# Performance work log

Hardware: AMD Instinct MI355X
Metric: run time of the kernel (lower is better)

## Reference

```python
import jax, jax.numpy as jnp
import numpy as np

N_NODES = 50000
KEEP_PROB = 0.5  # dropout = 0.5


def setup_inputs() -> dict:
    key = jax.random.key(0)
    k1, k2, k3, k4, k5 = jax.random.split(key, 5)
    S, E, DIN, DOUT = 2, 800000, 512, 128
    x = jax.random.normal(k1, (N_NODES, DIN), dtype=jnp.float32)
    weights = jax.random.normal(k2, (S, DIN, DOUT), dtype=jnp.float32) * (1.0 / np.sqrt(DIN))
    adj_rows = jax.random.randint(k3, (S, E), 0, N_NODES, dtype=jnp.int32)
    adj_cols = jax.random.randint(k4, (S, E), 0, N_NODES, dtype=jnp.int32)
    adj_vals = jax.random.uniform(k5, (S, E), dtype=jnp.float32)
    return {"x": x, "weights": weights, "adj_rows": adj_rows,
            "adj_cols": adj_cols, "adj_vals": adj_vals}


def reference(x, weights, adj_rows, adj_cols, adj_vals):
    # Dropout (TF semantics: mask and scale by 1/keep_prob), fixed key for determinism.
    mask = (jax.random.uniform(jax.random.key(42), x.shape) < KEEP_PROB)
    xd = x * mask.astype(x.dtype) / KEEP_PROB
    # Dense GEMM per support: pre_sup[s] = dropout(x) @ W_s  -> [S, N, Dout]
    pre_sup = jnp.einsum('nd,sdo->sno', xd, weights)
    # SpMM per support: out[s] = A_s @ pre_sup[s] with A_s in COO form.
    def spmm(rows, cols, vals, h):
        return jax.ops.segment_sum(vals[:, None] * h[cols], rows,
                                   num_segments=N_NODES)
    out = jax.vmap(spmm)(adj_rows, adj_cols, adj_vals, pre_sup)  # [S, N, Dout]
    return jax.nn.relu(out)
```

## Files before the change

kernel.cpp:

```cpp
#include <hip/hip_runtime.h>
#include <stdint.h>

#define N_NODES 50000
#define DIN     512
#define DOUT    128
#define NSUP    2
#define EDGES   800000
#define NEDGE   (NSUP * EDGES)
#define NROWS   (NSUP * N_NODES)
#define NB      782
#define CH      8192
#define NCH     ((NEDGE + CH - 1) / CH)
#define EPT     16
#define SCAP    4096
#define NMASKW  ((N_NODES * DIN) / 32)
#define NMB     1563
#define NWC     256

typedef __attribute__((ext_vector_type(8))) short short8;
typedef __attribute__((ext_vector_type(4))) float f32x4;

__device__ __forceinline__ uint32_t rotl32(uint32_t v, uint32_t d) {
  return (v << d) | (v >> (32u - d));
}

__device__ __forceinline__ void threefry2x32(uint32_t x0, uint32_t x1,
                                             uint32_t& o0, uint32_t& o1) {
  const uint32_t ks0 = 0u;
  const uint32_t ks1 = 42u;
  const uint32_t ks2 = 0u ^ 42u ^ 0x1BD11BDAu;
  x0 += ks0; x1 += ks1;
#define TF_R(r) { x0 += x1; x1 = rotl32(x1, (r)); x1 ^= x0; }
  TF_R(13) TF_R(15) TF_R(26) TF_R(6)
  x0 += ks1; x1 += ks2 + 1u;
  TF_R(17) TF_R(29) TF_R(16) TF_R(24)
  x0 += ks2; x1 += ks0 + 2u;
  TF_R(13) TF_R(15) TF_R(26) TF_R(6)
  x0 += ks0; x1 += ks1 + 3u;
  TF_R(17) TF_R(29) TF_R(16) TF_R(24)
  x0 += ks1; x1 += ks2 + 4u;
  TF_R(13) TF_R(15) TF_R(26) TF_R(6)
  x0 += ks2; x1 += ks0 + 5u;
#undef TF_R
  o0 = x0; o1 = x1;
}

__device__ __forceinline__ bool keep_mask(uint32_t idx) {
  uint32_t o0, o1;
  threefry2x32(0u, idx, o0, o1);
  return ((o0 ^ o1) >> 31) == 0u;
}

__device__ __forceinline__ uint32_t pack_bf16x2(float a, float b) {
  uint32_t ua = __float_as_uint(a), ub = __float_as_uint(b);
  ua += 0x7fffu + ((ua >> 16) & 1u);
  ub += 0x7fffu + ((ub >> 16) & 1u);
  return (ua >> 16) | (ub & 0xffff0000u);
}

__device__ __forceinline__ uint32_t bf16rne(float f) {
  uint32_t u = __float_as_uint(f);
  u += 0x7fffu + ((u >> 16) & 1u);
  return u >> 16;
}

__global__ __launch_bounds__(512) void fused_pre(
    const int* __restrict__ rows, const float* __restrict__ w,
    uint32_t* __restrict__ maskbuf, int* __restrict__ gcnt,
    unsigned short* __restrict__ b16t) {
  const int t  = threadIdx.x;
  const int bb = blockIdx.x;
  if (bb < NCH) {
    __shared__ int hist[NB];
    for (int b = t; b < NB; b += 512) hist[b] = 0;
    __syncthreads();
    int e0 = bb * CH;
#pragma unroll
    for (int i = 0; i < EPT; ++i) {
      int e = e0 + i * 512 + t;
      if (e < NEDGE) {
        int s = (e >= EDGES) ? 1 : 0;
        int grow = s * N_NODES + rows[e];
        atomicAdd(&hist[grow >> 7], 1);
      }
    }
    __syncthreads();
    for (int b = t; b < NB; b += 512)
      if (hist[b]) atomicAdd(&gcnt[b], hist[b]);
  } else if (bb < NCH + NMB) {
    int wid = (bb - NCH) * 512 + t;
    if (wid < NMASKW) {
      uint32_t base = (uint32_t)wid * 32u;
      uint32_t m = 0u;
#pragma unroll 8
      for (int j = 0; j < 32; ++j)
        m |= (keep_mask(base + j) ? 1u : 0u) << j;
      maskbuf[wid] = m;
    }
  } else {
    int i = (bb - NCH - NMB) * 512 + t;
    if (i < NSUP * DIN * DOUT) {
      int s   = i >> 16;
      int rem = i & 65535;
      int k   = rem >> 7;
      int o   = rem & 127;
      b16t[(size_t)(s * DOUT + o) * DIN + k] = (unsigned short)bf16rne(w[i]);
    }
  }
}

__global__ __launch_bounds__(512) void gemm_mfma2(
    const float* __restrict__ x, const uint32_t* __restrict__ maskbuf,
    const unsigned short* __restrict__ b16t,
    unsigned short* __restrict__ pre16) {
  __shared__ unsigned short As[128 * 64];
  __shared__ unsigned short Bs[256 * 64];
  const int t    = threadIdx.x;
  const int lane = t & 63;
  const int w    = t >> 6;
  const int wr   = w >> 2;
  const int wc   = w & 3;
  const int m0   = blockIdx.x * 128;

  f32x4 acc[4][4];
#pragma unroll
  for (int i = 0; i < 4; ++i)
#pragma unroll
    for (int j = 0; j < 4; ++j) acc[i][j] = (f32x4){0.f, 0.f, 0.f, 0.f};

  for (int kc = 0; kc < DIN; kc += 64) {
    __syncthreads();
#pragma unroll
    for (int i = 0; i < 2; ++i) {
      int slot = i * 512 + t;
      int row  = slot >> 3;
      int k8   = (slot & 7) * 8;
      int grow = m0 + row;
      union { uint32_t u[4]; short8 s; } pk;
      if (grow < N_NODES) {
        uint32_t b8 = (uint32_t)grow * DIN + (uint32_t)(kc + k8);
        const float4* src = reinterpret_cast<const float4*>(x + b8);
        float4 v0 = src[0], v1 = src[1];
        float f[8] = {v0.x, v0.y, v0.z, v0.w, v1.x, v1.y, v1.z, v1.w};
        uint32_t bits = maskbuf[b8 >> 5] >> (b8 & 31u);
#pragma unroll
        for (int q = 0; q < 8; ++q)
          f[q] = ((bits >> q) & 1u) ? f[q] * 2.0f : 0.0f;
#pragma unroll
        for (int q = 0; q < 4; ++q) pk.u[q] = pack_bf16x2(f[2 * q], f[2 * q + 1]);
      } else {
#pragma unroll
        for (int q = 0; q < 4; ++q) pk.u[q] = 0u;
      }
      *reinterpret_cast<short8*>(&As[(row * 64 + k8) ^ ((row & 7) << 3)]) = pk.s;
    }
#pragma unroll
    for (int i = 0; i < 4; ++i) {
      int slot = i * 512 + t;
      int col  = slot >> 3;
      int k8   = (slot & 7) * 8;
      short8 v = *reinterpret_cast<const short8*>(
          b16t + (size_t)col * DIN + kc + k8);
      *reinterpret_cast<short8*>(&Bs[(col * 64 + k8) ^ ((col & 7) << 3)]) = v;
    }
    __syncthreads();

    short8 af[4][2], bf[2][4];
#pragma unroll
    for (int mf = 0; mf < 4; ++mf)
#pragma unroll
      for (int kk = 0; kk < 2; ++kk) {
        int row = wr * 64 + mf * 16 + (lane & 15);
        int idx = (row * 64 + kk * 32 + (lane >> 4) * 8) ^ ((row & 7) << 3);
        af[mf][kk] = *reinterpret_cast<const short8*>(&As[idx]);
      }
#pragma unroll
    for (int kk = 0; kk < 2; ++kk)
#pragma unroll
      for (int nf = 0; nf < 4; ++nf) {
        int col = wc * 64 + nf * 16 + (lane & 15);
        int idx = (col * 64 + kk * 32 + (lane >> 4) * 8) ^ ((col & 7) << 3);
        bf[kk][nf] = *reinterpret_cast<const short8*>(&Bs[idx]);
      }
#pragma unroll
    for (int mf = 0; mf < 4; ++mf)
#pragma unroll
      for (int nf = 0; nf < 4; ++nf)
#pragma unroll
        for (int kk = 0; kk < 2; ++kk)
          acc[mf][nf] = __builtin_amdgcn_mfma_f32_16x16x32_bf16(
              af[mf][kk], bf[kk][nf], acc[mf][nf], 0, 0, 0);
  }

#pragma unroll
  for (int mf = 0; mf < 4; ++mf) {
    int rbase = m0 + wr * 64 + mf * 16 + ((lane >> 4) * 4);
#pragma unroll
    for (int nf = 0; nf < 4; ++nf) {
      int col = wc * 64 + nf * 16 + (lane & 15);
      int s = col >> 7, o = col & 127;
#pragma unroll
      for (int q = 0; q < 4; ++q) {
        int row = rbase + q;
        if (row < N_NODES)
          pre16[(size_t)(s * N_NODES + row) * DOUT + o] =
              (unsigned short)bf16rne(acc[mf][nf][q]);
      }
    }
  }
}

__global__ __launch_bounds__(1024) void scan782(const int* __restrict__ gcnt,
                                                int* __restrict__ bstart,
                                                int* __restrict__ gcursor) {
  __shared__ int sm[1024];
  int t = threadIdx.x;
  int c = (t < NB) ? gcnt[t] : 0;
  sm[t] = c;
  __syncthreads();
  for (int d = 1; d < 1024; d <<= 1) {
    int v = sm[t];
    int a = (t >= d) ? sm[t - d] : 0;
    __syncthreads();
    sm[t] = v + a;
    __syncthreads();
  }
  if (t < NB) {
    int ex = sm[t] - c;
    bstart[t] = ex;
    gcursor[t] = ex;
  }
  if (t == NB - 1) bstart[NB] = sm[t];
}

__global__ __launch_bounds__(512) void bin_scatter(
    const int* __restrict__ rows, const int* __restrict__ cols,
    const float* __restrict__ vals, int* __restrict__ gcursor,
    uint64_t* __restrict__ binned) {
  __shared__ uint32_t hist[NB];
  __shared__ uint32_t hexcl[NB];
  __shared__ uint32_t sbase[NB];
  __shared__ uint32_t scanb[512];
  __shared__ uint64_t ordered[CH];
  __shared__ uint16_t bk16[CH];
  int t = threadIdx.x;
  for (int b = t; b < NB; b += 512) hist[b] = 0;
  __syncthreads();
  int e0 = blockIdx.x * CH;
  uint32_t key[EPT], rank[EPT], bkt[EPT], vbits[EPT];
#pragma unroll
  for (int i = 0; i < EPT; ++i) {
    int e = e0 + i * 512 + t;
    if (e < NEDGE) {
      int s = (e >= EDGES) ? 1 : 0;
      uint32_t grow = (uint32_t)(s * N_NODES + rows[e]);
      uint32_t gcol = (uint32_t)(s * N_NODES + cols[e]);
      vbits[i] = __float_as_uint(vals[e]);
      uint32_t b = grow >> 7;
      bkt[i] = b;
      key[i] = ((grow & 127u) << 17) | gcol;
      rank[i] = atomicAdd(&hist[b], 1u);
    } else {
      bkt[i] = 0xFFFFFFFFu;
    }
  }
  __syncthreads();
  int t2 = t * 2;
  uint32_t a0 = (t2 < NB) ? hist[t2] : 0u;
  uint32_t a1 = (t2 + 1 < NB) ? hist[t2 + 1] : 0u;
  scanb[t] = a0 + a1;
  __syncthreads();
  for (int d = 1; d < 512; d <<= 1) {
    uint32_t v = scanb[t];
    uint32_t a = (t >= d) ? scanb[t - d] : 0u;
    __syncthreads();
    scanb[t] = v + a;
    __syncthreads();
  }
  uint32_t base  = t ? scanb[t - 1] : 0u;
  uint32_t total = scanb[511];
  if (t2 < NB)     hexcl[t2]     = base;
  if (t2 + 1 < NB) hexcl[t2 + 1] = base + a0;
  for (int b = t; b < NB; b += 512)
    if (hist[b]) sbase[b] = (uint32_t)atomicAdd(&gcursor[b], (int)hist[b]);
  __syncthreads();
#pragma unroll
  for (int i = 0; i < EPT; ++i) {
    if (bkt[i] != 0xFFFFFFFFu) {
      uint32_t slot = hexcl[bkt[i]] + rank[i];
      ordered[slot] = ((uint64_t)vbits[i] << 32) | key[i];
      bk16[slot] = (uint16_t)bkt[i];
    }
  }
  __syncthreads();
#pragma unroll
  for (int i = 0; i < EPT; ++i) {
    uint32_t slot = (uint32_t)(i * 512 + t);
    if (slot < total) {
      uint32_t b = bk16[slot];
      uint32_t dst = sbase[b] + (slot - hexcl[b]);
      binned[dst] = ordered[slot];
    }
  }
}

__global__ __launch_bounds__(512) void spmm_sort_pull(
    const int* __restrict__ bstart, const uint64_t* __restrict__ binned,
    const uint32_t* __restrict__ preu, float* __restrict__ out) {
  __shared__ uint64_t ordered[SCAP];
  __shared__ uint32_t hist[128];
  __shared__ uint32_t excl[128];
  const int t = threadIdx.x;
  const int b = blockIdx.x;
  const int beg = bstart[b], end = bstart[b + 1];
  const int cnt = end - beg;
  if (t < 128) hist[t] = 0;
  __syncthreads();
  uint64_t ed[8];
  uint32_t rk[8], rw[8];
#pragma unroll
  for (int i = 0; i < 8; ++i) {
    int slot = i * 512 + t;
    if (slot < cnt) {
      uint64_t e = binned[beg + slot];
      ed[i] = e;
      uint32_t rowin = ((uint32_t)e >> 17) & 127u;
      rw[i] = rowin;
      rk[i] = atomicAdd(&hist[rowin], 1u);
    } else {
      rw[i] = 0xFFFFFFFFu;
    }
  }
  __syncthreads();
  if (t < 128) excl[t] = hist[t];
  __syncthreads();
  for (int d = 1; d < 128; d <<= 1) {
    uint32_t v = (t < 128) ? excl[t] : 0u;
    uint32_t a = (t >= d && t < 128) ? excl[t - d] : 0u;
    __syncthreads();
    if (t < 128) excl[t] = v + a;
    __syncthreads();
  }
  if (t < 128) excl[t] -= hist[t];
  __syncthreads();
#pragma unroll
  for (int i = 0; i < 8; ++i)
    if (rw[i] != 0xFFFFFFFFu)
      ordered[excl[rw[i]] + rk[i]] = ed[i];
  __syncthreads();

  const int lane = t & 63, wave = t >> 6;
  for (int r8 = 0; r8 < 16; ++r8) {
    int r = wave * 16 + r8;
    int grow = b * 128 + r;
    if (grow >= NROWS) break;
    int jbeg = excl[r];
    int jend = jbeg + (int)hist[r];
    float a0 = 0.f, a1 = 0.f;
    int j = jbeg;
    for (; j + 4 <= jend; j += 4) {
      uint64_t e0 = ordered[j],     e1 = ordered[j + 1];
      uint64_t e2 = ordered[j + 2], e3 = ordered[j + 3];
      uint32_t q0 = preu[(size_t)((uint32_t)e0 & 0x1FFFFu) * 64 + lane];
      uint32_t q1 = preu[(size_t)((uint32_t)e1 & 0x1FFFFu) * 64 + lane];
      uint32_t q2 = preu[(size_t)((uint32_t)e2 & 0x1FFFFu) * 64 + lane];
      uint32_t q3 = preu[(size_t)((uint32_t)e3 & 0x1FFFFu) * 64 + lane];
      float v0 = __uint_as_float((uint32_t)(e0 >> 32));
      float v1 = __uint_as_float((uint32_t)(e1 >> 32));
      float v2 = __uint_as_float((uint32_t)(e2 >> 32));
      float v3 = __uint_as_float((uint32_t)(e3 >> 32));
      a0 += v0 * __uint_as_float(q0 << 16);
      a1 += v0 * __uint_as_float(q0 & 0xffff0000u);
      a0 += v1 * __uint_as_float(q1 << 16);
      a1 += v1 * __uint_as_float(q1 & 0xffff0000u);
      a0 += v2 * __uint_as_float(q2 << 16);
      a1 += v2 * __uint_as_float(q2 & 0xffff0000u);
      a0 += v3 * __uint_as_float(q3 << 16);
      a1 += v3 * __uint_as_float(q3 & 0xffff0000u);
    }
    for (; j < jend; ++j) {
      uint64_t e = ordered[j];
      uint32_t q = preu[(size_t)((uint32_t)e & 0x1FFFFu) * 64 + lane];
      float v = __uint_as_float((uint32_t)(e >> 32));
      a0 += v * __uint_as_float(q << 16);
      a1 += v * __uint_as_float(q & 0xffff0000u);
    }
    float2 o = make_float2(fmaxf(a0, 0.f), fmaxf(a1, 0.f));
    *reinterpret_cast<float2*>(out + (size_t)grow * DOUT + 2 * lane) = o;
  }
}

extern "C" void kernel_launch(void* const* d_in, const int* in_sizes, int n_in,
                              void* d_out, int out_size, void* d_ws, size_t ws_size,
                              hipStream_t stream) {
  const float* x    = (const float*)d_in[0];
  const float* w    = (const float*)d_in[1];
  const int*   rows = (const int*)d_in[2];
  const int*   cols = (const int*)d_in[3];
  const float* vals = (const float*)d_in[4];
  float* out = (float*)d_out;

  uint32_t* base = (uint32_t*)d_ws;
  uint32_t* preu       = base;
  unsigned short* b16t = (unsigned short*)(base + 6400000);
  uint32_t* maskbuf    = base + 6400000 + 65536;
  int* gcnt      = (int*)(base + 6400000 + 65536 + 800000);
  int* bstart    = gcnt + 800;
  int* gcursor   = bstart + 800;
  uint64_t* binned = (uint64_t*)(gcursor + 800);
  size_t need = ((size_t)6400000 + 65536 + 800000 + 2400 + 3200000) * 4;
  if (ws_size < need) return;

  hipMemsetAsync(gcnt, 0, NB * sizeof(int), stream);

  fused_pre<<<NCH + NMB + NWC, 512, 0, stream>>>(rows, w, maskbuf, gcnt, b16t);
  scan782<<<1, 1024, 0, stream>>>(gcnt, bstart, gcursor);
  bin_scatter<<<NCH, 512, 0, stream>>>(rows, cols, vals, gcursor, binned);

  gemm_mfma2<<<(N_NODES + 127) / 128, 512, 0, stream>>>(x, maskbuf, b16t,
                                                        (unsigned short*)preu);

  spmm_sort_pull<<<NB, 512, 0, stream>>>(bstart, binned, preu, out);
}
```

Baseline: 196.0 us.

## Halve GEMM M-tile and prefetch next K-chunk into registers

The dense dropout GEMM now uses a 64-row M-tile instead of 128, so twice as many blocks are launched, and each wave covers 32 output columns across all 64 rows. Global loads for the next K-chunk of x, the mask bits and the weights are issued into registers before the MFMA work on the current chunk, so memory latency overlaps with compute. The trade-off is more weight tile traffic per output row, since B is re-read by twice as many blocks, plus extra register pressure from the prefetch buffers.

```diff
diff --git a/kernel.cpp b/kernel.cpp
--- a/kernel.cpp
+++ b/kernel.cpp
@@ -109,95 +109,117 @@
   }
 }
 
-__global__ __launch_bounds__(512) void gemm_mfma2(
+__global__ __launch_bounds__(512) void gemm_mfma3(
     const float* __restrict__ x, const uint32_t* __restrict__ maskbuf,
     const unsigned short* __restrict__ b16t,
     unsigned short* __restrict__ pre16) {
-  __shared__ unsigned short As[128 * 64];
+  __shared__ unsigned short As[64 * 64];
   __shared__ unsigned short Bs[256 * 64];
   const int t    = threadIdx.x;
   const int lane = t & 63;
-  const int w    = t >> 6;
-  const int wr   = w >> 2;
-  const int wc   = w & 3;
-  const int m0   = blockIdx.x * 128;
-
-  f32x4 acc[4][4];
+  const int wc   = t >> 6;
+  const int m0   = blockIdx.x * 64;
+
+  f32x4 acc[4][2];
 #pragma unroll
   for (int i = 0; i < 4; ++i)
 #pragma unroll
-    for (int j = 0; j < 4; ++j) acc[i][j] = (f32x4){0.f, 0.f, 0.f, 0.f};
-
-  for (int kc = 0; kc < DIN; kc += 64) {
-    __syncthreads();
-#pragma unroll
-    for (int i = 0; i < 2; ++i) {
-      int slot = i * 512 + t;
-      int row  = slot >> 3;
-      int k8   = (slot & 7) * 8;
-      int grow = m0 + row;
+    for (int j = 0; j < 2; ++j) acc[i][j] = (f32x4){0.f, 0.f, 0.f, 0.f};
+
+  const int arow  = t >> 3;
+  const int ak8   = (t & 7) * 8;
+  const int agrow = m0 + arow;
+  const bool avalid = agrow < N_NODES;
+  const uint32_t abase = (uint32_t)agrow * DIN + (uint32_t)ak8;
+  const int aswz  = (arow * 64 + ak8) ^ ((arow & 7) << 3);
+
+  float4 pa0, pa1;
+  uint32_t pm = 0u;
+  short8 pb[4];
+
+#define LOADCH(KC)                                                         \
+  {                                                                        \
+    if (avalid) {                                                          \
+      const float4* s_ = reinterpret_cast<const float4*>(x + abase + (KC)); \
+      pa0 = s_[0];                                                         \
+      pa1 = s_[1];                                                         \
+      uint32_t b8_ = abase + (uint32_t)(KC);                               \
+      pm = maskbuf[b8_ >> 5] >> (b8_ & 31u);                               \
+    }                                                                      \
+    _Pragma("unroll")                                                      \
+    for (int i_ = 0; i_ < 4; ++i_) {                                       \
+      int slot_ = i_ * 512 + t;                                            \
+      int col_  = slot_ >> 3;                                              \
+      int k8_   = (slot_ & 7) * 8;                                         \
+      pb[i_] = *reinterpret_cast<const short8*>(                           \
+          b16t + (size_t)col_ * DIN + (KC) + k8_);                         \
+    }                                                                      \
+  }
+
+  LOADCH(0);
+
+  for (int kc8 = 0; kc8 < 8; ++kc8) {
+    const int kc = kc8 * 64;
+    __syncthreads();
+    {
       union { uint32_t u[4]; short8 s; } pk;
-      if (grow < N_NODES) {
-        uint32_t b8 = (uint32_t)grow * DIN + (uint32_t)(kc + k8);
-        const float4* src = reinterpret_cast<const float4*>(x + b8);
-        float4 v0 = src[0], v1 = src[1];
-        float f[8] = {v0.x, v0.y, v0.z, v0.w, v1.x, v1.y, v1.z, v1.w};
-        uint32_t bits = maskbuf[b8 >> 5] >> (b8 & 31u);
+      if (avalid) {
+        float f[8] = {pa0.x, pa0.y, pa0.z, pa0.w, pa1.x, pa1.y, pa1.z, pa1.w};
 #pragma unroll
         for (int q = 0; q < 8; ++q)
-          f[q] = ((bits >> q) & 1u) ? f[q] * 2.0f : 0.0f;
+          f[q] = ((pm >> q) & 1u) ? f[q] * 2.0f : 0.0f;
 #pragma unroll
         for (int q = 0; q < 4; ++q) pk.u[q] = pack_bf16x2(f[2 * q], f[2 * q + 1]);
       } else {
 #pragma unroll
         for (int q = 0; q < 4; ++q) pk.u[q] = 0u;
       }
-      *reinterpret_cast<short8*>(&As[(row * 64 + k8) ^ ((row & 7) << 3)]) = pk.s;
+      *reinterpret_cast<short8*>(&As[aswz]) = pk.s;
     }
 #pragma unroll
     for (int i = 0; i < 4; ++i) {
       int slot = i * 512 + t;
       int col  = slot >> 3;
       int k8   = (slot & 7) * 8;
-      short8 v = *reinterpret_cast<const short8*>(
-          b16t + (size_t)col * DIN + kc + k8);
-      *reinterpret_cast<short8*>(&Bs[(col * 64 + k8) ^ ((col & 7) << 3)]) = v;
-    }
-    __syncthreads();
-
-    short8 af[4][2], bf[2][4];
+      *reinterpret_cast<short8*>(&Bs[(col * 64 + k8) ^ ((col & 7) << 3)]) = pb[i];
+    }
+    if (kc8 < 7) LOADCH(kc + 64);
+    __syncthreads();
+
+    short8 af[4][2], bf[2][2];
 #pragma unroll
     for (int mf = 0; mf < 4; ++mf)
 #pragma unroll
       for (int kk = 0; kk < 2; ++kk) {
-        int row = wr * 64 + mf * 16 + (lane & 15);
+        int row = mf * 16 + (lane & 15);
         int idx = (row * 64 + kk * 32 + (lane >> 4) * 8) ^ ((row & 7) << 3);
         af[mf][kk] = *reinterpret_cast<const short8*>(&As[idx]);
       }
 #pragma unroll
     for (int kk = 0; kk < 2; ++kk)
 #pragma unroll
-      for (int nf = 0; nf < 4; ++nf) {
-        int col = wc * 64 + nf * 16 + (lane & 15);
+      for (int nf = 0; nf < 2; ++nf) {
+        int col = wc * 32 + nf * 16 + (lane & 15);
         int idx = (col * 64 + kk * 32 + (lane >> 4) * 8) ^ ((col & 7) << 3);
         bf[kk][nf] = *reinterpret_cast<const short8*>(&Bs[idx]);
       }
 #pragma unroll
     for (int mf = 0; mf < 4; ++mf)
 #pragma unroll
-      for (int nf = 0; nf < 4; ++nf)
+      for (int nf = 0; nf < 2; ++nf)
 #pragma unroll
         for (int kk = 0; kk < 2; ++kk)
           acc[mf][nf] = __builtin_amdgcn_mfma_f32_16x16x32_bf16(
               af[mf][kk], bf[kk][nf], acc[mf][nf], 0, 0, 0);
   }
+#undef LOADCH
 
 #pragma unroll
   for (int mf = 0; mf < 4; ++mf) {
-    int rbase = m0 + wr * 64 + mf * 16 + ((lane >> 4) * 4);
-#pragma unroll
-    for (int nf = 0; nf < 4; ++nf) {
-      int col = wc * 64 + nf * 16 + (lane & 15);
+    int rbase = m0 + mf * 16 + ((lane >> 4) * 4);
+#pragma unroll
+    for (int nf = 0; nf < 2; ++nf) {
+      int col = wc * 32 + nf * 16 + (lane & 15);
       int s = col >> 7, o = col & 127;
 #pragma unroll
       for (int q = 0; q < 4; ++q) {
@@ -417,8 +439,8 @@
   scan782<<<1, 1024, 0, stream>>>(gcnt, bstart, gcursor);
   bin_scatter<<<NCH, 512, 0, stream>>>(rows, cols, vals, gcursor, binned);
 
-  gemm_mfma2<<<(N_NODES + 127) / 128, 512, 0, stream>>>(x, maskbuf, b16t,
-                                                        (unsigned short*)preu);
+  gemm_mfma3<<<(N_NODES + 63) / 64, 512, 0, stream>>>(x, maskbuf, b16t,
+                                                      (unsigned short*)preu);
 
   spmm_sort_pull<<<NB, 512, 0, stream>>>(bstart, binned, preu, out);
 }
```

Result: faster. 191.4 us (median of 2 runs) (-2.4%).

## Restructure dropout GEMM with register-direct A and async LDS loads for B

Applied to the files above, without the earlier changes.

Replaces the 128x256 GEMM block with a 64-row, 4-wave block. Each wave loads its own 16 rows of x straight into registers, double-buffered one k-chunk ahead, and applies the dropout mask and bf16 conversion there, so the A tile no longer goes through shared memory. B is copied into LDS with global_load_lds using explicit waitcnt and barrier control, so loads overlap the MFMA work. This frees LDS traffic and adds prefetch overlap, at the cost of more register pressure (16 accumulators plus prefetch buffers), each block re-reading the full B tile, and fragile hand-tuned wait counts.

```diff
diff --git a/kernel.cpp b/kernel.cpp
--- a/kernel.cpp
+++ b/kernel.cpp
@@ -109,103 +109,112 @@
   }
 }
 
-__global__ __launch_bounds__(512) void gemm_mfma2(
+__device__ __forceinline__ short8 conv8(float4 a, float4 b, uint32_t bits) {
+  float f[8] = {a.x, a.y, a.z, a.w, b.x, b.y, b.z, b.w};
+  union { uint32_t u[4]; short8 s; } pk;
+#pragma unroll
+  for (int q = 0; q < 8; ++q)
+    f[q] = ((bits >> q) & 1u) ? f[q] * 2.0f : 0.0f;
+#pragma unroll
+  for (int q = 0; q < 4; ++q) pk.u[q] = pack_bf16x2(f[2 * q], f[2 * q + 1]);
+  return pk.s;
+}
+
+__global__ __launch_bounds__(256) void gemm_mfma5(
     const float* __restrict__ x, const uint32_t* __restrict__ maskbuf,
     const unsigned short* __restrict__ b16t,
     unsigned short* __restrict__ pre16) {
-  __shared__ unsigned short As[128 * 64];
   __shared__ unsigned short Bs[256 * 64];
   const int t    = threadIdx.x;
   const int lane = t & 63;
   const int w    = t >> 6;
-  const int wr   = w >> 2;
-  const int wc   = w & 3;
-  const int m0   = blockIdx.x * 128;
-
-  f32x4 acc[4][4];
-#pragma unroll
-  for (int i = 0; i < 4; ++i)
-#pragma unroll
-    for (int j = 0; j < 4; ++j) acc[i][j] = (f32x4){0.f, 0.f, 0.f, 0.f};
-
-  for (int kc = 0; kc < DIN; kc += 64) {
-    __syncthreads();
-#pragma unroll
-    for (int i = 0; i < 2; ++i) {
-      int slot = i * 512 + t;
-      int row  = slot >> 3;
-      int k8   = (slot & 7) * 8;
-      int grow = m0 + row;
-      union { uint32_t u[4]; short8 s; } pk;
-      if (grow < N_NODES) {
-        uint32_t b8 = (uint32_t)grow * DIN + (uint32_t)(kc + k8);
-        const float4* src = reinterpret_cast<const float4*>(x + b8);
-        float4 v0 = src[0], v1 = src[1];
-        float f[8] = {v0.x, v0.y, v0.z, v0.w, v1.x, v1.y, v1.z, v1.w};
-        uint32_t bits = maskbuf[b8 >> 5] >> (b8 & 31u);
-#pragma unroll
-        for (int q = 0; q < 8; ++q)
-          f[q] = ((bits >> q) & 1u) ? f[q] * 2.0f : 0.0f;
-#pragma unroll
-        for (int q = 0; q < 4; ++q) pk.u[q] = pack_bf16x2(f[2 * q], f[2 * q + 1]);
-      } else {
-#pragma unroll
-        for (int q = 0; q < 4; ++q) pk.u[q] = 0u;
-      }
-      *reinterpret_cast<short8*>(&As[(row * 64 + k8) ^ ((row & 7) << 3)]) = pk.s;
-    }
-#pragma unroll
-    for (int i = 0; i < 4; ++i) {
-      int slot = i * 512 + t;
-      int col  = slot >> 3;
-      int k8   = (slot & 7) * 8;
-      short8 v = *reinterpret_cast<const short8*>(
-          b16t + (size_t)col * DIN + kc + k8);
-      *reinterpret_cast<short8*>(&Bs[(col * 64 + k8) ^ ((col & 7) << 3)]) = v;
-    }
-    __syncthreads();
-
-    short8 af[4][2], bf[2][4];
-#pragma unroll
-    for (int mf = 0; mf < 4; ++mf)
-#pragma unroll
-      for (int kk = 0; kk < 2; ++kk) {
-        int row = wr * 64 + mf * 16 + (lane & 15);
-        int idx = (row * 64 + kk * 32 + (lane >> 4) * 8) ^ ((row & 7) << 3);
-        af[mf][kk] = *reinterpret_cast<const short8*>(&As[idx]);
-      }
-#pragma unroll
-    for (int kk = 0; kk < 2; ++kk)
-#pragma unroll
-      for (int nf = 0; nf < 4; ++nf) {
-        int col = wc * 64 + nf * 16 + (lane & 15);
-        int idx = (col * 64 + kk * 32 + (lane >> 4) * 8) ^ ((col & 7) << 3);
-        bf[kk][nf] = *reinterpret_cast<const short8*>(&Bs[idx]);
-      }
-#pragma unroll
-    for (int mf = 0; mf < 4; ++mf)
-#pragma unroll
-      for (int nf = 0; nf < 4; ++nf)
-#pragma unroll
-        for (int kk = 0; kk < 2; ++kk)
-          acc[mf][nf] = __builtin_amdgcn_mfma_f32_16x16x32_bf16(
-              af[mf][kk], bf[kk][nf], acc[mf][nf], 0, 0, 0);
-  }
-
-#pragma unroll
-  for (int mf = 0; mf < 4; ++mf) {
-    int rbase = m0 + wr * 64 + mf * 16 + ((lane >> 4) * 4);
-#pragma unroll
-    for (int nf = 0; nf < 4; ++nf) {
-      int col = wc * 64 + nf * 16 + (lane & 15);
-      int s = col >> 7, o = col & 127;
-#pragma unroll
-      for (int q = 0; q < 4; ++q) {
-        int row = rbase + q;
-        if (row < N_NODES)
-          pre16[(size_t)(s * N_NODES + row) * DOUT + o] =
-              (unsigned short)bf16rne(acc[mf][nf][q]);
-      }
+  const int m0   = blockIdx.x * 64;
+  const int rowa = m0 + w * 16 + (lane & 15);
+  const int rowc = rowa < N_NODES ? rowa : N_NODES - 1;
+  const int k8   = (lane >> 4) * 8;
+  const float* xrow = x + (size_t)rowc * DIN;
+  const int mrow = rowc * 16;
+
+  f32x4 acc[16];
+#pragma unroll
+  for (int i = 0; i < 16; ++i) acc[i] = (f32x4){0.f, 0.f, 0.f, 0.f};
+
+  float4 pa[2][2][2];
+  uint32_t pmw[2][2];
+
+  const int colb = w * 64 + (lane >> 3);
+  const uint32_t ksw = (uint32_t)(((lane & 7) ^ (lane >> 3)) << 3);
+
+#define LOADA(KC, S)                                                          \
+  {                                                                           \
+    const float4* a0_ = reinterpret_cast<const float4*>(xrow + (KC) + k8);    \
+    pa[S][0][0] = a0_[0];                                                     \
+    pa[S][0][1] = a0_[1];                                                     \
+    const float4* a1_ =                                                       \
+        reinterpret_cast<const float4*>(xrow + (KC) + 32 + k8);               \
+    pa[S][1][0] = a1_[0];                                                     \
+    pa[S][1][1] = a1_[1];                                                     \
+    pmw[S][0] = maskbuf[mrow + ((KC) >> 5)];                                  \
+    pmw[S][1] = maskbuf[mrow + ((KC) >> 5) + 1];                              \
+  }
+
+  LOADA(0, 0);
+
+#pragma unroll
+  for (int kc8 = 0; kc8 < 8; ++kc8) {
+    const int kc = kc8 * 64;
+    asm volatile("s_waitcnt lgkmcnt(0)" ::: "memory");
+    __builtin_amdgcn_s_barrier();
+#pragma unroll
+    for (int i = 0; i < 8; ++i) {
+      const unsigned short* g =
+          b16t + (size_t)(colb + i * 8) * DIN + kc + ksw;
+      __builtin_amdgcn_global_load_lds((const void*)g,
+                                       (void*)(&Bs[w * 4096 + i * 512]),
+                                       16, 0, 0);
+    }
+    __builtin_amdgcn_sched_barrier(0);
+    if (kc8 < 7) {
+      if ((kc8 & 1) == 0) { LOADA(kc + 64, 1); }
+      else                { LOADA(kc + 64, 0); }
+    }
+    __builtin_amdgcn_sched_barrier(0);
+    if (kc8 < 7) { asm volatile("s_waitcnt vmcnt(5)" ::: "memory"); }
+    else         { asm volatile("s_waitcnt vmcnt(0)" ::: "memory"); }
+    __builtin_amdgcn_s_barrier();
+
+    short8 a0, a1;
+    if ((kc8 & 1) == 0) {
+      a0 = conv8(pa[0][0][0], pa[0][0][1], pmw[0][0] >> k8);
+      a1 = conv8(pa[0][1][0], pa[0][1][1], pmw[0][1] >> k8);
+    } else {
+      a0 = conv8(pa[1][0][0], pa[1][0][1], pmw[1][0] >> k8);
+      a1 = conv8(pa[1][1][0], pa[1][1][1], pmw[1][1] >> k8);
+    }
+#pragma unroll
+    for (int nf = 0; nf < 16; ++nf) {
+      int col  = nf * 16 + (lane & 15);
+      int base = col * 64 + ((lane >> 4) * 8);
+      int sw   = (col & 7) << 3;
+      short8 b0 = *reinterpret_cast<const short8*>(&Bs[base ^ sw]);
+      short8 b1 = *reinterpret_cast<const short8*>(&Bs[(base + 32) ^ sw]);
+      acc[nf] = __builtin_amdgcn_mfma_f32_16x16x32_bf16(a0, b0, acc[nf], 0, 0, 0);
+      acc[nf] = __builtin_amdgcn_mfma_f32_16x16x32_bf16(a1, b1, acc[nf], 0, 0, 0);
+    }
+  }
+#undef LOADA
+
+  const int rb = m0 + w * 16 + ((lane >> 4) * 4);
+#pragma unroll
+  for (int nf = 0; nf < 16; ++nf) {
+    int col = nf * 16 + (lane & 15);
+    int s = col >> 7, o = col & 127;
+#pragma unroll
+    for (int q = 0; q < 4; ++q) {
+      int row = rb + q;
+      if (row < N_NODES)
+        pre16[(size_t)(s * N_NODES + row) * DOUT + o] =
+            (unsigned short)bf16rne(acc[nf][q]);
     }
   }
 }
@@ -417,8 +426,8 @@
   scan782<<<1, 1024, 0, stream>>>(gcnt, bstart, gcursor);
   bin_scatter<<<NCH, 512, 0, stream>>>(rows, cols, vals, gcursor, binned);
 
-  gemm_mfma2<<<(N_NODES + 127) / 128, 512, 0, stream>>>(x, maskbuf, b16t,
-                                                        (unsigned short*)preu);
+  gemm_mfma5<<<(N_NODES + 63) / 64, 256, 0, stream>>>(x, maskbuf, b16t,
+                                                      (unsigned short*)preu);
 
   spmm_sort_pull<<<NB, 512, 0, stream>>>(bstart, binned, preu, out);
 }
```

Result: no change. 193.0 us (-1.5%).
